# Kernel optimization log

Hardware: AMD Instinct MI355X
Metric: run time of the kernel (lower is better)

The kernel has to match this reference:

```python
import jax, jax.numpy as jnp
import numpy as np

N = 10000      # num_nodes
E = 640000     # num_edges
D = 256        # in_channels
POOL_SIZES = [(N, 48), (48, 12), (12, 4), (4, 1)]


def gcn_conv(x, src, dst, ew, W, b, n):
    """PyG-style GCNConv with edge weights: add self-loops, symmetric norm, scatter-add."""
    loop = jnp.arange(n)
    s = jnp.concatenate([src, loop])
    d = jnp.concatenate([dst, loop])
    w = jnp.concatenate([ew, jnp.ones((n,), x.dtype)])
    deg = jax.ops.segment_sum(w, d, num_segments=n)
    dinv = jnp.where(deg > 0, deg ** -0.5, 0.0)
    norm = dinv[s] * w * dinv[d]                      # [E+N]
    h = x @ W                                         # [n, out]
    out = jax.ops.segment_sum(norm[:, None] * h[s], d, num_segments=n)
    return out + b


def diffpool(x, P):
    """Learned-assignment DiffPool: S=softmax(P); x'=S^T x; reg = mean row entropy of S."""
    S = jax.nn.softmax(P, axis=-1)                    # [n_in, n_out]
    xp = S.T @ x                                      # [n_out, feat]
    reg = jnp.mean(-jnp.sum(S * jnp.log(S + 1e-12), axis=-1))
    return xp, reg


def setup_inputs() -> dict:
    key = jax.random.key(0)
    ks = jax.random.split(key, 12)
    inp = {
        "x": jax.random.normal(ks[0], (N, D), jnp.float32),
        "edge_index": jax.random.randint(ks[1], (2, E), 0, N, jnp.int64),
        "edge_attr": jax.random.uniform(ks[2], (E, 1), jnp.float32),
        "adj": jax.random.uniform(ks[3], (N, N), jnp.float32),
        # GCNConv params (out channels hard-coded to 1 in the module)
        "W1": jax.random.normal(ks[4], (D, 1), jnp.float32) / np.sqrt(D),
        "b1": jnp.zeros((1,), jnp.float32),
        "W2": jax.random.normal(ks[5], (1, 1), jnp.float32),
        "b2": jnp.zeros((1,), jnp.float32),
    }
    for i, (ni, no) in enumerate(POOL_SIZES):
        inp[f"P{i+1}"] = jax.random.normal(ks[6 + i], (ni, no), jnp.float32) * 0.1
    return inp


def reference(x, edge_index, edge_attr, adj, W1, b1, W2, b2, P1, P2, P3, P4):
    src, dst = edge_index[0], edge_index[1]
    ew = edge_attr[:, 0]
    h1 = gcn_conv(x, src, dst, ew, W1, b1, N)                       # [N,1]
    h = jnp.concatenate([h1, gcn_conv(h1[:, -1:], src, dst, ew, W2, b2, N)], axis=-1)
    h = jnp.concatenate([h, gcn_conv(h[:, -1:], src, dst, ew, W2, b2, N)], axis=-1)  # [N,3]
    reg = jnp.float32(0.0)
    for P in (P1, P2, P3, P4):
        h, r = diffpool(h, P)
        reg = reg + r
    return (h, reg)                                                  # h: [1,3]
```

## Files before the change

kernel.cpp:

```cpp
#include <hip/hip_runtime.h>
#include <math.h>

#define NN 10000
#define EE 640000
#define DD 256
#define SB 256
#define EPB (EE / SB)
#define NTHR 512
#define RB 157

#define OFF_DINV 0
#define OFF_XW   (NN)
#define OFF_C1   (2*NN)
#define OFF_C2   (3*NN)
#define OFF_U0   (4*NN)
#define OFF_U1   (5*NN)
#define OFF_U2   (6*NN)
#define OFF_XP   (7*NN)
#define OFF_PART (7*NN + 160)

__global__ __launch_bounds__(NTHR) void k1_deg_xw(
    const int* __restrict__ dst, const float* __restrict__ ew,
    const float* __restrict__ x, const float* __restrict__ W1,
    float* __restrict__ ws)
{
    __shared__ float acc[NN];
    int tid = threadIdx.x, bid = blockIdx.x;
    int lane = tid & 63, wv = tid >> 6;
    if (bid == 0 && tid < 160) ws[OFF_XP + tid] = 0.f;
    for (int i = tid; i < NN; i += NTHR) acc[i] = 0.f;
    __syncthreads();
    {
        float4 wreg = reinterpret_cast<const float4*>(W1)[lane];
        float* xw = ws + OFF_XW;
        for (int row = bid * 8 + wv; row < NN; row += SB * 8) {
            float4 a = reinterpret_cast<const float4*>(x + (size_t)row * DD)[lane];
            float v = a.x*wreg.x + a.y*wreg.y + a.z*wreg.z + a.w*wreg.w;
            #pragma unroll
            for (int off = 32; off; off >>= 1) v += __shfl_xor(v, off);
            if (lane == 0) xw[row] = v;
        }
    }
    int base = bid * EPB;
    for (int k = tid; k < EPB; k += NTHR) {
        int e = base + k;
        atomicAdd(&acc[dst[e]], ew[e]);
    }
    __syncthreads();
    float* p = ws + OFF_PART + (size_t)bid * NN;
    for (int i = tid; i < NN; i += NTHR) p[i] = acc[i];
}

__global__ __launch_bounds__(NTHR) void k2_dinv(float* __restrict__ ws)
{
    __shared__ float red[8][64];
    int tid = threadIdx.x, bid = blockIdx.x;
    int nl = tid & 63, sl = tid >> 6;
    int node = bid * 64 + nl;
    const float* part = ws + OFF_PART;
    float s = 0.f;
    if (node < NN) {
        #pragma unroll 8
        for (int it = 0; it < SB / 8; ++it)
            s += part[(size_t)(sl * (SB / 8) + it) * NN + node];
    }
    red[sl][nl] = s;
    __syncthreads();
    if (tid < 64 && node < NN) {
        float tot = 1.f;
        #pragma unroll
        for (int q = 0; q < 8; ++q) tot += red[q][tid];
        float di = (tot > 0.f) ? 1.0f / sqrtf(tot) : 0.f;
        ws[OFF_DINV + node] = di;
        ws[OFF_U0 + node] = di * ws[OFF_XW + node];
    }
}

__global__ __launch_bounds__(NTHR) void k_scat(
    const int* __restrict__ src, const int* __restrict__ dst,
    const float* __restrict__ ew, const float* __restrict__ u,
    float* __restrict__ ws)
{
    __shared__ float acc[NN];
    int tid = threadIdx.x, bid = blockIdx.x;
    for (int i = tid; i < NN; i += NTHR) acc[i] = 0.f;
    __syncthreads();
    int base = bid * EPB;
    for (int k = tid; k < EPB; k += NTHR) {
        int e = base + k;
        atomicAdd(&acc[dst[e]], ew[e] * u[src[e]]);
    }
    __syncthreads();
    float* p = ws + OFF_PART + (size_t)bid * NN;
    for (int i = tid; i < NN; i += NTHR) p[i] = acc[i];
}

__global__ __launch_bounds__(NTHR) void k_red_conv(
    const float* __restrict__ hin, const float* __restrict__ multp,
    const float* __restrict__ biasp, float* __restrict__ cout,
    float* __restrict__ uout, float* __restrict__ ws)
{
    __shared__ float red[8][64];
    int tid = threadIdx.x, bid = blockIdx.x;
    int nl = tid & 63, sl = tid >> 6;
    int node = bid * 64 + nl;
    const float* part = ws + OFF_PART;
    float s = 0.f;
    if (node < NN) {
        #pragma unroll 8
        for (int it = 0; it < SB / 8; ++it)
            s += part[(size_t)(sl * (SB / 8) + it) * NN + node];
    }
    red[sl][nl] = s;
    __syncthreads();
    if (tid < 64 && node < NN) {
        float tot = 0.f;
        #pragma unroll
        for (int q = 0; q < 8; ++q) tot += red[q][tid];
        float di = ws[OFF_DINV + node];
        float M = multp ? *multp : 1.0f;
        float cv = M * di * (tot + di * hin[node]) + *biasp;
        cout[node] = cv;
        uout[node] = di * cv;
    }
}

__global__ __launch_bounds__(NTHR) void k8_final(
    const float* __restrict__ hin,
    const float* __restrict__ multp, const float* __restrict__ biasp,
    const float* __restrict__ c1, const float* __restrict__ c2,
    const float* __restrict__ P1, const float* __restrict__ P2,
    const float* __restrict__ P3, float* __restrict__ ws, float* __restrict__ out)
{
    __shared__ float red[8][64];
    __shared__ float s_c3[64];
    __shared__ float part[8][48][3];
    __shared__ float entW[8];
    __shared__ int sh_last;
    int tid = threadIdx.x, bid = blockIdx.x;
    int lane = tid & 63, wv = tid >> 6;
    int node = bid * 64 + lane;
    const float* partg = ws + OFF_PART;
    float s = 0.f;
    if (node < NN) {
        #pragma unroll 8
        for (int it = 0; it < SB / 8; ++it)
            s += partg[(size_t)(wv * (SB / 8) + it) * NN + node];
    }
    red[wv][lane] = s;
    __syncthreads();
    if (tid < 64) {
        float cv = 0.f;
        if (node < NN) {
            float tot = 0.f;
            #pragma unroll
            for (int q = 0; q < 8; ++q) tot += red[q][tid];
            float di = ws[OFF_DINV + node];
            cv = (*multp) * di * (tot + di * hin[node]) + *biasp;
        }
        s_c3[tid] = cv;
    }
    __syncthreads();
    float a0 = 0.f, a1 = 0.f, a2 = 0.f, ent = 0.f;
    for (int j = 0; j < 8; ++j) {
        int rl = wv * 8 + j;
        int row = bid * 64 + rl;
        if (row >= NN) break;
        float v = (lane < 48) ? P1[(size_t)row * 48 + lane] : -1e30f;
        float mx = v;
        #pragma unroll
        for (int off = 32; off; off >>= 1) mx = fmaxf(mx, __shfl_xor(mx, off));
        float e = (lane < 48) ? expf(v - mx) : 0.f;
        float sum = e;
        #pragma unroll
        for (int off = 32; off; off >>= 1) sum += __shfl_xor(sum, off);
        float p = e / sum;
        if (lane < 48) {
            ent -= p * logf(p + 1e-12f);
            a0 += p * c1[row];
            a1 += p * c2[row];
            a2 += p * s_c3[rl];
        }
    }
    #pragma unroll
    for (int off = 32; off; off >>= 1) ent += __shfl_xor(ent, off);
    if (lane == 0) entW[wv] = ent;
    if (lane < 48) { part[wv][lane][0] = a0; part[wv][lane][1] = a1; part[wv][lane][2] = a2; }
    __syncthreads();
    float* xp1 = ws + OFF_XP;
    if (tid < 144) {
        int j = tid / 3, col = tid % 3;
        float sp = 0.f;
        #pragma unroll
        for (int w = 0; w < 8; ++w) sp += part[w][j][col];
        atomicAdd(&xp1[j * 3 + col], sp);
    }
    if (tid == 0) {
        float sp = 0.f;
        #pragma unroll
        for (int w = 0; w < 8; ++w) sp += entW[w];
        atomicAdd(&xp1[144], sp);
    }
    if (tid == 0) {
        __threadfence();
        int old = atomicAdd((int*)ws + OFF_XP + 152, 1);
        sh_last = (old == (int)gridDim.x - 1) ? 1 : 0;
    }
    __syncthreads();
    if (sh_last) {
        __shared__ float shXp[145];
        __shared__ float S2[48][12], xp2[12][3];
        __shared__ float S3[12][4], xp3[4][3];
        __shared__ float ent2, ent3;
        if (tid < 145) shXp[tid] = atomicAdd(&xp1[tid], 0.0f);
        if (tid == 0) { ent2 = 0.f; ent3 = 0.f; }
        __syncthreads();
        if (tid < 48) {
            float v[12], mx = -1e30f;
            #pragma unroll
            for (int j = 0; j < 12; j++) { v[j] = P2[tid * 12 + j]; mx = fmaxf(mx, v[j]); }
            float sm = 0.f;
            #pragma unroll
            for (int j = 0; j < 12; j++) { v[j] = expf(v[j] - mx); sm += v[j]; }
            float e = 0.f;
            #pragma unroll
            for (int j = 0; j < 12; j++) {
                float p = v[j] / sm; S2[tid][j] = p; e -= p * logf(p + 1e-12f);
            }
            atomicAdd(&ent2, e);
        }
        __syncthreads();
        if (tid < 36) {
            int j = tid / 3, col = tid % 3;
            float sm = 0.f;
            for (int i = 0; i < 48; i++) sm += S2[i][j] * shXp[i * 3 + col];
            xp2[j][col] = sm;
        }
        __syncthreads();
        if (tid < 12) {
            float v[4], mx = -1e30f;
            #pragma unroll
            for (int j = 0; j < 4; j++) { v[j] = P3[tid * 4 + j]; mx = fmaxf(mx, v[j]); }
            float sm = 0.f;
            #pragma unroll
            for (int j = 0; j < 4; j++) { v[j] = expf(v[j] - mx); sm += v[j]; }
            float e = 0.f;
            #pragma unroll
            for (int j = 0; j < 4; j++) {
                float p = v[j] / sm; S3[tid][j] = p; e -= p * logf(p + 1e-12f);
            }
            atomicAdd(&ent3, e);
        }
        __syncthreads();
        if (tid < 12) {
            int j = tid / 3, col = tid % 3;
            float sm = 0.f;
            for (int i = 0; i < 12; i++) sm += S3[i][j] * xp2[i][col];
            xp3[j][col] = sm;
        }
        __syncthreads();
        if (tid == 0) {
            float o0 = 0.f, o1 = 0.f, o2 = 0.f;
            for (int i = 0; i < 4; i++) {
                o0 += xp3[i][0]; o1 += xp3[i][1]; o2 += xp3[i][2];
            }
            float reg = shXp[144] / (float)NN + ent2 / 48.f + ent3 / 12.f;
            out[0] = o0; out[1] = o1; out[2] = o2; out[3] = reg;
        }
    }
}

extern "C" void kernel_launch(void* const* d_in, const int* in_sizes, int n_in,
                              void* d_out, int out_size, void* d_ws, size_t ws_size,
                              hipStream_t stream) {
    const float* x  = (const float*)d_in[0];
    const int*   ei = (const int*)d_in[1];
    const float* ea = (const float*)d_in[2];
    const float* W1 = (const float*)d_in[4];
    const float* b1 = (const float*)d_in[5];
    const float* W2 = (const float*)d_in[6];
    const float* b2 = (const float*)d_in[7];
    const float* P1 = (const float*)d_in[8];
    const float* P2 = (const float*)d_in[9];
    const float* P3 = (const float*)d_in[10];
    const int* src = ei;
    const int* dst = ei + EE;
    float* ws  = (float*)d_ws;
    float* out = (float*)d_out;

    k1_deg_xw<<<SB, NTHR, 0, stream>>>(dst, ea, x, W1, ws);
    k2_dinv<<<RB, NTHR, 0, stream>>>(ws);
    k_scat<<<SB, NTHR, 0, stream>>>(src, dst, ea, ws + OFF_U0, ws);
    k_red_conv<<<RB, NTHR, 0, stream>>>(ws + OFF_XW, nullptr, b1,
                                        ws + OFF_C1, ws + OFF_U1, ws);
    k_scat<<<SB, NTHR, 0, stream>>>(src, dst, ea, ws + OFF_U1, ws);
    k_red_conv<<<RB, NTHR, 0, stream>>>(ws + OFF_C1, W2, b2,
                                        ws + OFF_C2, ws + OFF_U2, ws);
    k_scat<<<SB, NTHR, 0, stream>>>(src, dst, ea, ws + OFF_U2, ws);
    k8_final<<<RB, NTHR, 0, stream>>>(ws + OFF_C2, W2, b2,
                                      ws + OFF_C1, ws + OFF_C2,
                                      P1, P2, P3, ws, out);
}
```

Measured before the change: 87.05 us.

## Fuse all GCN and DiffPool phases into one persistent kernel with grid barriers

Replaces the eight separate kernel launches with a single persistent kernel of 256 blocks. The phases are separated by software grid barriers built on atomic counters, and one memset zeroes the accumulators and counters. The reduction phases now cover 40 nodes per block so all 256 blocks take part, and block 0 runs the final small pooling stages after a last barrier. This removes launch gaps and inter-kernel drains, but relies on all 256 blocks being co-resident (a barrier can deadlock otherwise) and adds spin-wait barrier overhead.

```diff
diff --git a/kernel.cpp b/kernel.cpp
--- a/kernel.cpp
+++ b/kernel.cpp
@@ -4,10 +4,10 @@
 #define NN 10000
 #define EE 640000
 #define DD 256
-#define SB 256
-#define EPB (EE / SB)
+#define NBLK 256
 #define NTHR 512
-#define RB 157
+#define EPB (EE / NBLK)
+#define NPB 40
 
 #define OFF_DINV 0
 #define OFF_XW   (NN)
@@ -19,200 +19,213 @@
 #define OFF_XP   (7*NN)
 #define OFF_PART (7*NN + 160)
 
-__global__ __launch_bounds__(NTHR) void k1_deg_xw(
+__device__ __forceinline__ void gbar(int* c) {
+    __syncthreads();
+    if (threadIdx.x == 0) {
+        __hip_atomic_fetch_add(c, 1, __ATOMIC_ACQ_REL, __HIP_MEMORY_SCOPE_AGENT);
+        while (__hip_atomic_load(c, __ATOMIC_RELAXED, __HIP_MEMORY_SCOPE_AGENT) < NBLK)
+            __builtin_amdgcn_s_sleep(1);
+        __builtin_amdgcn_fence(__ATOMIC_ACQUIRE, "agent");
+    }
+    __syncthreads();
+}
+
+__global__ __launch_bounds__(NTHR) void mega2(
+    const float* __restrict__ x, const int* __restrict__ src,
     const int* __restrict__ dst, const float* __restrict__ ew,
-    const float* __restrict__ x, const float* __restrict__ W1,
-    float* __restrict__ ws)
-{
-    __shared__ float acc[NN];
-    int tid = threadIdx.x, bid = blockIdx.x;
-    int lane = tid & 63, wv = tid >> 6;
-    if (bid == 0 && tid < 160) ws[OFF_XP + tid] = 0.f;
-    for (int i = tid; i < NN; i += NTHR) acc[i] = 0.f;
-    __syncthreads();
-    {
-        float4 wreg = reinterpret_cast<const float4*>(W1)[lane];
-        float* xw = ws + OFF_XW;
-        for (int row = bid * 8 + wv; row < NN; row += SB * 8) {
-            float4 a = reinterpret_cast<const float4*>(x + (size_t)row * DD)[lane];
-            float v = a.x*wreg.x + a.y*wreg.y + a.z*wreg.z + a.w*wreg.w;
-            #pragma unroll
-            for (int off = 32; off; off >>= 1) v += __shfl_xor(v, off);
-            if (lane == 0) xw[row] = v;
-        }
-    }
-    int base = bid * EPB;
-    for (int k = tid; k < EPB; k += NTHR) {
-        int e = base + k;
-        atomicAdd(&acc[dst[e]], ew[e]);
-    }
-    __syncthreads();
-    float* p = ws + OFF_PART + (size_t)bid * NN;
-    for (int i = tid; i < NN; i += NTHR) p[i] = acc[i];
-}
-
-__global__ __launch_bounds__(NTHR) void k2_dinv(float* __restrict__ ws)
-{
-    __shared__ float red[8][64];
-    int tid = threadIdx.x, bid = blockIdx.x;
-    int nl = tid & 63, sl = tid >> 6;
-    int node = bid * 64 + nl;
-    const float* part = ws + OFF_PART;
-    float s = 0.f;
-    if (node < NN) {
-        #pragma unroll 8
-        for (int it = 0; it < SB / 8; ++it)
-            s += part[(size_t)(sl * (SB / 8) + it) * NN + node];
-    }
-    red[sl][nl] = s;
-    __syncthreads();
-    if (tid < 64 && node < NN) {
-        float tot = 1.f;
-        #pragma unroll
-        for (int q = 0; q < 8; ++q) tot += red[q][tid];
-        float di = (tot > 0.f) ? 1.0f / sqrtf(tot) : 0.f;
-        ws[OFF_DINV + node] = di;
-        ws[OFF_U0 + node] = di * ws[OFF_XW + node];
-    }
-}
-
-__global__ __launch_bounds__(NTHR) void k_scat(
-    const int* __restrict__ src, const int* __restrict__ dst,
-    const float* __restrict__ ew, const float* __restrict__ u,
-    float* __restrict__ ws)
-{
-    __shared__ float acc[NN];
-    int tid = threadIdx.x, bid = blockIdx.x;
-    for (int i = tid; i < NN; i += NTHR) acc[i] = 0.f;
-    __syncthreads();
-    int base = bid * EPB;
-    for (int k = tid; k < EPB; k += NTHR) {
-        int e = base + k;
-        atomicAdd(&acc[dst[e]], ew[e] * u[src[e]]);
-    }
-    __syncthreads();
-    float* p = ws + OFF_PART + (size_t)bid * NN;
-    for (int i = tid; i < NN; i += NTHR) p[i] = acc[i];
-}
-
-__global__ __launch_bounds__(NTHR) void k_red_conv(
-    const float* __restrict__ hin, const float* __restrict__ multp,
-    const float* __restrict__ biasp, float* __restrict__ cout,
-    float* __restrict__ uout, float* __restrict__ ws)
-{
-    __shared__ float red[8][64];
-    int tid = threadIdx.x, bid = blockIdx.x;
-    int nl = tid & 63, sl = tid >> 6;
-    int node = bid * 64 + nl;
-    const float* part = ws + OFF_PART;
-    float s = 0.f;
-    if (node < NN) {
-        #pragma unroll 8
-        for (int it = 0; it < SB / 8; ++it)
-            s += part[(size_t)(sl * (SB / 8) + it) * NN + node];
-    }
-    red[sl][nl] = s;
-    __syncthreads();
-    if (tid < 64 && node < NN) {
-        float tot = 0.f;
-        #pragma unroll
-        for (int q = 0; q < 8; ++q) tot += red[q][tid];
-        float di = ws[OFF_DINV + node];
-        float M = multp ? *multp : 1.0f;
-        float cv = M * di * (tot + di * hin[node]) + *biasp;
-        cout[node] = cv;
-        uout[node] = di * cv;
-    }
-}
-
-__global__ __launch_bounds__(NTHR) void k8_final(
-    const float* __restrict__ hin,
-    const float* __restrict__ multp, const float* __restrict__ biasp,
-    const float* __restrict__ c1, const float* __restrict__ c2,
+    const float* __restrict__ W1, const float* __restrict__ b1v,
+    const float* __restrict__ W2v, const float* __restrict__ b2v,
     const float* __restrict__ P1, const float* __restrict__ P2,
     const float* __restrict__ P3, float* __restrict__ ws, float* __restrict__ out)
 {
+    __shared__ float acc[NN];
     __shared__ float red[8][64];
-    __shared__ float s_c3[64];
+    __shared__ float s_c3[NPB];
     __shared__ float part[8][48][3];
     __shared__ float entW[8];
-    __shared__ int sh_last;
-    int tid = threadIdx.x, bid = blockIdx.x;
-    int lane = tid & 63, wv = tid >> 6;
-    int node = bid * 64 + lane;
-    const float* partg = ws + OFF_PART;
-    float s = 0.f;
-    if (node < NN) {
-        #pragma unroll 8
-        for (int it = 0; it < SB / 8; ++it)
-            s += partg[(size_t)(wv * (SB / 8) + it) * NN + node];
-    }
-    red[wv][lane] = s;
+
+    const int tid = threadIdx.x, bid = blockIdx.x;
+    const int lane = tid & 63, wv = tid >> 6;
+    const int ebase = bid * EPB;
+    const int node = bid * NPB + lane;
+    const bool nok = (lane < NPB) && (node < NN);
+
+    float* dinv_g = ws + OFF_DINV;
+    float* xw_g   = ws + OFF_XW;
+    float* c1_g   = ws + OFF_C1;
+    float* c2_g   = ws + OFF_C2;
+    float* xp1    = ws + OFF_XP;
+    int*   ctr    = (int*)(ws + OFF_XP + 148);
+    float* part_g = ws + OFF_PART;
+    float* pmy    = part_g + (size_t)bid * NN;
+
+    const float b1s = *b1v, b2s = *b2v, W2s = *W2v;
+
+    for (int i = tid; i < NN; i += NTHR) acc[i] = 0.f;
+    {
+        float4 wreg = reinterpret_cast<const float4*>(W1)[lane];
+        for (int row = bid * 8 + wv; row < NN; row += NBLK * 8) {
+            float4 a = reinterpret_cast<const float4*>(x + (size_t)row * DD)[lane];
+            float v = a.x*wreg.x + a.y*wreg.y + a.z*wreg.z + a.w*wreg.w;
+            #pragma unroll
+            for (int off = 32; off; off >>= 1) v += __shfl_xor(v, off);
+            if (lane == 0) xw_g[row] = v;
+        }
+    }
     __syncthreads();
-    if (tid < 64) {
-        float cv = 0.f;
-        if (node < NN) {
-            float tot = 0.f;
-            #pragma unroll
-            for (int q = 0; q < 8; ++q) tot += red[q][tid];
-            float di = ws[OFF_DINV + node];
-            cv = (*multp) * di * (tot + di * hin[node]) + *biasp;
-        }
-        s_c3[tid] = cv;
+    for (int k = tid; k < EPB; k += NTHR) {
+        int e = ebase + k;
+        atomicAdd(&acc[dst[e]], ew[e]);
     }
     __syncthreads();
-    float a0 = 0.f, a1 = 0.f, a2 = 0.f, ent = 0.f;
-    for (int j = 0; j < 8; ++j) {
-        int rl = wv * 8 + j;
-        int row = bid * 64 + rl;
-        if (row >= NN) break;
-        float v = (lane < 48) ? P1[(size_t)row * 48 + lane] : -1e30f;
-        float mx = v;
+    for (int i = tid; i < NN; i += NTHR) pmy[i] = acc[i];
+    gbar(&ctr[0]);
+
+    {
+        int sl = wv;
+        float s = 0.f;
+        if (nok) {
+            #pragma unroll 8
+            for (int it = 0; it < 32; ++it)
+                s += part_g[(size_t)(sl * 32 + it) * NN + node];
+        }
+        red[sl][lane] = s;
+        __syncthreads();
+        if (wv == 0 && nok) {
+            float tot = 1.f;
+            #pragma unroll
+            for (int q = 0; q < 8; ++q) tot += red[q][lane];
+            float di = (tot > 0.f) ? 1.0f / sqrtf(tot) : 0.f;
+            dinv_g[node] = di;
+            ws[OFF_U0 + node] = di * xw_g[node];
+        }
+    }
+    gbar(&ctr[1]);
+
+#define SCAT_PHASE(UOFF)                                              \
+    for (int i = tid; i < NN; i += NTHR) acc[i] = 0.f;                \
+    __syncthreads();                                                  \
+    for (int k = tid; k < EPB; k += NTHR) {                           \
+        int e = ebase + k;                                            \
+        atomicAdd(&acc[dst[e]], ew[e] * ws[(UOFF) + src[e]]);         \
+    }                                                                 \
+    __syncthreads();                                                  \
+    for (int i = tid; i < NN; i += NTHR) pmy[i] = acc[i];
+
+#define RED_PHASE(HING, M, B, COUTG, UOFF_OUT)                        \
+    {                                                                 \
+        int sl = wv;                                                  \
+        float s = 0.f;                                                \
+        if (nok) {                                                    \
+            _Pragma("unroll 8")                                       \
+            for (int it = 0; it < 32; ++it)                           \
+                s += part_g[(size_t)(sl * 32 + it) * NN + node];      \
+        }                                                             \
+        red[sl][lane] = s;                                            \
+        __syncthreads();                                              \
+        if (wv == 0 && nok) {                                         \
+            float tot = 0.f;                                          \
+            _Pragma("unroll")                                         \
+            for (int q = 0; q < 8; ++q) tot += red[q][lane];          \
+            float di = dinv_g[node];                                  \
+            float cv = (M) * di * (tot + di * (HING)[node]) + (B);    \
+            (COUTG)[node] = cv;                                       \
+            ws[(UOFF_OUT) + node] = di * cv;                          \
+        }                                                             \
+    }
+
+    SCAT_PHASE(OFF_U0)
+    gbar(&ctr[2]);
+    RED_PHASE(xw_g, 1.0f, b1s, c1_g, OFF_U1)
+    gbar(&ctr[3]);
+
+    SCAT_PHASE(OFF_U1)
+    gbar(&ctr[4]);
+    RED_PHASE(c1_g, W2s, b2s, c2_g, OFF_U2)
+    gbar(&ctr[5]);
+
+    SCAT_PHASE(OFF_U2)
+    gbar(&ctr[6]);
+
+    {
+        int sl = wv;
+        float s = 0.f;
+        if (nok) {
+            #pragma unroll 8
+            for (int it = 0; it < 32; ++it)
+                s += part_g[(size_t)(sl * 32 + it) * NN + node];
+        }
+        red[sl][lane] = s;
+        __syncthreads();
+        if (wv == 0 && lane < NPB) {
+            float cv = 0.f;
+            if (node < NN) {
+                float tot = 0.f;
+                #pragma unroll
+                for (int q = 0; q < 8; ++q) tot += red[q][lane];
+                float di = dinv_g[node];
+                cv = W2s * di * (tot + di * c2_g[node]) + b2s;
+            }
+            s_c3[lane] = cv;
+        }
+        __syncthreads();
+    }
+    {
+        float a0 = 0.f, a1 = 0.f, a2 = 0.f, ent = 0.f;
         #pragma unroll
-        for (int off = 32; off; off >>= 1) mx = fmaxf(mx, __shfl_xor(mx, off));
-        float e = (lane < 48) ? expf(v - mx) : 0.f;
-        float sum = e;
+        for (int j = 0; j < 5; ++j) {
+            int rl = wv * 5 + j;
+            int row = bid * NPB + rl;
+            if (row < NN) {
+                float pv = (lane < 48) ? P1[(size_t)row * 48 + lane] : -1e30f;
+                float mx = pv;
+                #pragma unroll
+                for (int off = 32; off; off >>= 1) mx = fmaxf(mx, __shfl_xor(mx, off));
+                float e = (lane < 48) ? expf(pv - mx) : 0.f;
+                float sum = e;
+                #pragma unroll
+                for (int off = 32; off; off >>= 1) sum += __shfl_xor(sum, off);
+                float p = e / sum;
+                if (lane < 48) {
+                    ent -= p * logf(p + 1e-12f);
+                    a0 += p * c1_g[row];
+                    a1 += p * c2_g[row];
+                    a2 += p * s_c3[rl];
+                }
+            }
+        }
         #pragma unroll
-        for (int off = 32; off; off >>= 1) sum += __shfl_xor(sum, off);
-        float p = e / sum;
-        if (lane < 48) {
-            ent -= p * logf(p + 1e-12f);
-            a0 += p * c1[row];
-            a1 += p * c2[row];
-            a2 += p * s_c3[rl];
-        }
-    }
-    #pragma unroll
-    for (int off = 32; off; off >>= 1) ent += __shfl_xor(ent, off);
-    if (lane == 0) entW[wv] = ent;
-    if (lane < 48) { part[wv][lane][0] = a0; part[wv][lane][1] = a1; part[wv][lane][2] = a2; }
-    __syncthreads();
-    float* xp1 = ws + OFF_XP;
-    if (tid < 144) {
-        int j = tid / 3, col = tid % 3;
-        float sp = 0.f;
-        #pragma unroll
-        for (int w = 0; w < 8; ++w) sp += part[w][j][col];
-        atomicAdd(&xp1[j * 3 + col], sp);
-    }
-    if (tid == 0) {
-        float sp = 0.f;
-        #pragma unroll
-        for (int w = 0; w < 8; ++w) sp += entW[w];
-        atomicAdd(&xp1[144], sp);
-    }
-    if (tid == 0) {
-        __threadfence();
-        int old = atomicAdd((int*)ws + OFF_XP + 152, 1);
-        sh_last = (old == (int)gridDim.x - 1) ? 1 : 0;
-    }
-    __syncthreads();
-    if (sh_last) {
-        __shared__ float shXp[145];
+        for (int off = 32; off; off >>= 1) ent += __shfl_xor(ent, off);
+        if (lane == 0) entW[wv] = ent;
+        if (lane < 48) { part[wv][lane][0] = a0; part[wv][lane][1] = a1; part[wv][lane][2] = a2; }
+        __syncthreads();
+        if (tid < 144) {
+            int j = tid / 3, col = tid % 3;
+            float sp = 0.f;
+            #pragma unroll
+            for (int w = 0; w < 8; ++w) sp += part[w][j][col];
+            atomicAdd(&xp1[j * 3 + col], sp);
+        }
+        if (tid == 0) {
+            float sp = 0.f;
+            #pragma unroll
+            for (int w = 0; w < 8; ++w) sp += entW[w];
+            atomicAdd(&xp1[144], sp);
+        }
+    }
+
+    if (bid != 0) {
+        __syncthreads();
+        if (tid == 0)
+            __hip_atomic_fetch_add(&ctr[7], 1, __ATOMIC_RELEASE, __HIP_MEMORY_SCOPE_AGENT);
+        return;
+    }
+    gbar(&ctr[7]);
+
+    {
         __shared__ float S2[48][12], xp2[12][3];
         __shared__ float S3[12][4], xp3[4][3];
         __shared__ float ent2, ent3;
-        if (tid < 145) shXp[tid] = atomicAdd(&xp1[tid], 0.0f);
         if (tid == 0) { ent2 = 0.f; ent3 = 0.f; }
         __syncthreads();
         if (tid < 48) {
@@ -233,7 +246,7 @@
         if (tid < 36) {
             int j = tid / 3, col = tid % 3;
             float sm = 0.f;
-            for (int i = 0; i < 48; i++) sm += S2[i][j] * shXp[i * 3 + col];
+            for (int i = 0; i < 48; i++) sm += S2[i][j] * xp1[i * 3 + col];
             xp2[j][col] = sm;
         }
         __syncthreads();
@@ -264,7 +277,7 @@
             for (int i = 0; i < 4; i++) {
                 o0 += xp3[i][0]; o1 += xp3[i][1]; o2 += xp3[i][2];
             }
-            float reg = shXp[144] / (float)NN + ent2 / 48.f + ent3 / 12.f;
+            float reg = xp1[144] / (float)NN + ent2 / 48.f + ent3 / 12.f;
             out[0] = o0; out[1] = o1; out[2] = o2; out[3] = reg;
         }
     }
@@ -288,16 +301,7 @@
     float* ws  = (float*)d_ws;
     float* out = (float*)d_out;
 
-    k1_deg_xw<<<SB, NTHR, 0, stream>>>(dst, ea, x, W1, ws);
-    k2_dinv<<<RB, NTHR, 0, stream>>>(ws);
-    k_scat<<<SB, NTHR, 0, stream>>>(src, dst, ea, ws + OFF_U0, ws);
-    k_red_conv<<<RB, NTHR, 0, stream>>>(ws + OFF_XW, nullptr, b1,
-                                        ws + OFF_C1, ws + OFF_U1, ws);
-    k_scat<<<SB, NTHR, 0, stream>>>(src, dst, ea, ws + OFF_U1, ws);
-    k_red_conv<<<RB, NTHR, 0, stream>>>(ws + OFF_C1, W2, b2,
-                                        ws + OFF_C2, ws + OFF_U2, ws);
-    k_scat<<<SB, NTHR, 0, stream>>>(src, dst, ea, ws + OFF_U2, ws);
-    k8_final<<<RB, NTHR, 0, stream>>>(ws + OFF_C2, W2, b2,
-                                      ws + OFF_C1, ws + OFF_C2,
-                                      P1, P2, P3, ws, out);
+    hipMemsetAsync(ws + OFF_XP, 0, 160 * sizeof(float), stream);
+    mega2<<<NBLK, NTHR, 0, stream>>>(x, src, dst, ea, W1, b1, W2, b2,
+                                     P1, P2, P3, ws, out);
 }
```

Measured after the change: 198.7 us. 128% more time.

## Bucket edges by source block and fuse reductions into subsequent scatter kernels

Applied to the files above, without the earlier changes.

The first kernel now counting-sorts each edge chunk into 64 source-node buckets, packing the destination, local source index and weight into one 8-byte record. It also computes x@W1 and degree partials in the same pass. Each later kernel reduces the previous layer's partial sums for its own 157 nodes, computes the scaled source values in shared memory, and scatters only its bucket's edges. This cuts the launch count from eight to five and the partial-sum buffers from 256 to 64 copies. The cost is that the scatter phases run on only 64 blocks, each reading 256 small segments, which may underuse the GPU.

```diff
diff --git a/kernel.cpp b/kernel.cpp
--- a/kernel.cpp
+++ b/kernel.cpp
@@ -4,182 +4,208 @@
 #define NN 10000
 #define EE 640000
 #define DD 256
-#define SB 256
-#define EPB (EE / SB)
+#define NW 256
+#define EPW (EE / NW)
+#define NB 64
+#define NPB 157
 #define NTHR 512
-#define RB 157
+#define DEGB 64
+#define EPD (EE / DEGB)
 
 #define OFF_DINV 0
 #define OFF_XW   (NN)
 #define OFF_C1   (2*NN)
 #define OFF_C2   (3*NN)
-#define OFF_U0   (4*NN)
-#define OFF_U1   (5*NN)
-#define OFF_U2   (6*NN)
-#define OFF_XP   (7*NN)
-#define OFF_PART (7*NN + 160)
-
-__global__ __launch_bounds__(NTHR) void k1_deg_xw(
-    const int* __restrict__ dst, const float* __restrict__ ew,
-    const float* __restrict__ x, const float* __restrict__ W1,
-    float* __restrict__ ws)
-{
-    __shared__ float acc[NN];
+#define OFF_XP   (4*NN)
+#define OFF_BND  (4*NN + 160)
+#define OFF_S1   (OFF_BND + NW*65)
+#define OFF_DEGP (OFF_S1 + 2*EE)
+#define OFF_PART (OFF_DEGP + (size_t)DEGB*NN)
+
+__global__ __launch_bounds__(NTHR) void k1_sort_xw_deg(
+    const int* __restrict__ src, const int* __restrict__ dst,
+    const float* __restrict__ ew, const float* __restrict__ x,
+    const float* __restrict__ W1, float* __restrict__ ws)
+{
+    __shared__ int   sSrc[EPW], sDst[EPW];
+    __shared__ float sEw[EPW];
+    __shared__ int   cnt[NB], pf[NB + 1], curs[NB];
+    __shared__ float accD[NN];
     int tid = threadIdx.x, bid = blockIdx.x;
     int lane = tid & 63, wv = tid >> 6;
     if (bid == 0 && tid < 160) ws[OFF_XP + tid] = 0.f;
-    for (int i = tid; i < NN; i += NTHR) acc[i] = 0.f;
-    __syncthreads();
+    if (tid < NB) cnt[tid] = 0;
+    __syncthreads();
+    int base = bid * EPW;
+    for (int k = tid; k < EPW; k += NTHR) {
+        int s = src[base + k], d = dst[base + k];
+        sSrc[k] = s; sDst[k] = d; sEw[k] = ew[base + k];
+        atomicAdd(&cnt[s / NPB], 1);
+    }
+    __syncthreads();
+    if (tid < NB) {
+        int v = cnt[tid];
+        int incl = v;
+        #pragma unroll
+        for (int off = 1; off < 64; off <<= 1) {
+            int t = __shfl_up(incl, off);
+            if (lane >= off) incl += t;
+        }
+        int excl = incl - v;
+        pf[tid] = excl; curs[tid] = excl;
+        if (tid == NB - 1) pf[NB] = incl;
+    }
+    __syncthreads();
+    int* bndp = (int*)ws + OFF_BND;
+    if (tid < NB + 1) bndp[bid * 65 + tid] = pf[tid];
+    uint2* S1 = (uint2*)(ws + OFF_S1);
+    for (int k = tid; k < EPW; k += NTHR) {
+        int s = sSrc[k];
+        int j = s / NPB, loc = s - j * NPB;
+        int pos = atomicAdd(&curs[j], 1);
+        uint2 pk;
+        pk.x = (unsigned)sDst[k] | ((unsigned)loc << 14);
+        pk.y = __float_as_uint(sEw[k]);
+        S1[bid * EPW + pos] = pk;
+    }
     {
         float4 wreg = reinterpret_cast<const float4*>(W1)[lane];
-        float* xw = ws + OFF_XW;
-        for (int row = bid * 8 + wv; row < NN; row += SB * 8) {
-            float4 a = reinterpret_cast<const float4*>(x + (size_t)row * DD)[lane];
-            float v = a.x*wreg.x + a.y*wreg.y + a.z*wreg.z + a.w*wreg.w;
-            #pragma unroll
-            for (int off = 32; off; off >>= 1) v += __shfl_xor(v, off);
-            if (lane == 0) xw[row] = v;
-        }
-    }
-    int base = bid * EPB;
-    for (int k = tid; k < EPB; k += NTHR) {
-        int e = base + k;
-        atomicAdd(&acc[dst[e]], ew[e]);
-    }
-    __syncthreads();
-    float* p = ws + OFF_PART + (size_t)bid * NN;
-    for (int i = tid; i < NN; i += NTHR) p[i] = acc[i];
-}
-
-__global__ __launch_bounds__(NTHR) void k2_dinv(float* __restrict__ ws)
-{
-    __shared__ float red[8][64];
+        #pragma unroll
+        for (int r = 0; r < 5; ++r) {
+            int row = bid * 40 + wv * 5 + r;
+            if (row < NN) {
+                float4 a = reinterpret_cast<const float4*>(x + (size_t)row * DD)[lane];
+                float v = a.x*wreg.x + a.y*wreg.y + a.z*wreg.z + a.w*wreg.w;
+                #pragma unroll
+                for (int off = 32; off; off >>= 1) v += __shfl_xor(v, off);
+                if (lane == 0) ws[OFF_XW + row] = v;
+            }
+        }
+    }
+    if (bid < DEGB) {
+        for (int i = tid; i < NN; i += NTHR) accD[i] = 0.f;
+        __syncthreads();
+        int b2 = bid * EPD;
+        for (int k = tid; k < EPD; k += NTHR)
+            atomicAdd(&accD[dst[b2 + k]], ew[b2 + k]);
+        __syncthreads();
+        float* dp = ws + OFF_DEGP + (size_t)bid * NN;
+        for (int i = tid; i < NN; i += NTHR) dp[i] = accD[i];
+    }
+}
+
+__device__ __forceinline__ void bucket_scatter(
+    const int* bndp, const uint2* S1, const float* du, float* acc, int bid,
+    int lane, int wv)
+{
+    for (int w = wv; w < NW; w += 8) {
+        int s = bndp[w * 65 + bid], e = bndp[w * 65 + bid + 1];
+        for (int k = s + lane; k < e; k += 64) {
+            uint2 pk = S1[w * EPW + k];
+            atomicAdd(&acc[pk.x & 0x3FFF], __uint_as_float(pk.y) * du[pk.x >> 14]);
+        }
+    }
+}
+
+__global__ __launch_bounds__(NTHR) void k2_dinv_conv1(float* __restrict__ ws)
+{
+    __shared__ float acc[NN];
+    __shared__ float du[NPB];
     int tid = threadIdx.x, bid = blockIdx.x;
-    int nl = tid & 63, sl = tid >> 6;
-    int node = bid * 64 + nl;
-    const float* part = ws + OFF_PART;
-    float s = 0.f;
-    if (node < NN) {
-        #pragma unroll 8
-        for (int it = 0; it < SB / 8; ++it)
-            s += part[(size_t)(sl * (SB / 8) + it) * NN + node];
-    }
-    red[sl][nl] = s;
-    __syncthreads();
-    if (tid < 64 && node < NN) {
-        float tot = 1.f;
-        #pragma unroll
-        for (int q = 0; q < 8; ++q) tot += red[q][tid];
-        float di = (tot > 0.f) ? 1.0f / sqrtf(tot) : 0.f;
-        ws[OFF_DINV + node] = di;
-        ws[OFF_U0 + node] = di * ws[OFF_XW + node];
-    }
-}
-
-__global__ __launch_bounds__(NTHR) void k_scat(
-    const int* __restrict__ src, const int* __restrict__ dst,
-    const float* __restrict__ ew, const float* __restrict__ u,
+    int lane = tid & 63, wv = tid >> 6;
+    int nbase = bid * NPB;
+    int ncnt = min(NPB, NN - nbase);
+    for (int i = tid; i < NN; i += NTHR) acc[i] = 0.f;
+    if (tid < ncnt) {
+        float s = 1.f;
+        const float* dp = ws + OFF_DEGP;
+        for (int w = 0; w < DEGB; ++w) s += dp[(size_t)w * NN + nbase + tid];
+        float di = (s > 0.f) ? 1.0f / sqrtf(s) : 0.f;
+        ws[OFF_DINV + nbase + tid] = di;
+        du[tid] = di * ws[OFF_XW + nbase + tid];
+    }
+    __syncthreads();
+    bucket_scatter((const int*)ws + OFF_BND, (const uint2*)(ws + OFF_S1),
+                   du, acc, bid, lane, wv);
+    __syncthreads();
+    float* pp = ws + OFF_PART + (size_t)bid * NN;
+    for (int i = tid; i < NN; i += NTHR) pp[i] = acc[i];
+}
+
+__global__ __launch_bounds__(NTHR) void k_conv(
+    const float* __restrict__ hing, const float* __restrict__ multp,
+    const float* __restrict__ biasp, float* __restrict__ cout,
+    const float* __restrict__ pin, float* __restrict__ pout,
     float* __restrict__ ws)
 {
     __shared__ float acc[NN];
+    __shared__ float du[NPB];
     int tid = threadIdx.x, bid = blockIdx.x;
+    int lane = tid & 63, wv = tid >> 6;
+    int nbase = bid * NPB;
+    int ncnt = min(NPB, NN - nbase);
     for (int i = tid; i < NN; i += NTHR) acc[i] = 0.f;
-    __syncthreads();
-    int base = bid * EPB;
-    for (int k = tid; k < EPB; k += NTHR) {
-        int e = base + k;
-        atomicAdd(&acc[dst[e]], ew[e] * u[src[e]]);
-    }
-    __syncthreads();
-    float* p = ws + OFF_PART + (size_t)bid * NN;
-    for (int i = tid; i < NN; i += NTHR) p[i] = acc[i];
-}
-
-__global__ __launch_bounds__(NTHR) void k_red_conv(
-    const float* __restrict__ hin, const float* __restrict__ multp,
-    const float* __restrict__ biasp, float* __restrict__ cout,
-    float* __restrict__ uout, float* __restrict__ ws)
-{
-    __shared__ float red[8][64];
-    int tid = threadIdx.x, bid = blockIdx.x;
-    int nl = tid & 63, sl = tid >> 6;
-    int node = bid * 64 + nl;
-    const float* part = ws + OFF_PART;
-    float s = 0.f;
-    if (node < NN) {
-        #pragma unroll 8
-        for (int it = 0; it < SB / 8; ++it)
-            s += part[(size_t)(sl * (SB / 8) + it) * NN + node];
-    }
-    red[sl][nl] = s;
-    __syncthreads();
-    if (tid < 64 && node < NN) {
-        float tot = 0.f;
-        #pragma unroll
-        for (int q = 0; q < 8; ++q) tot += red[q][tid];
-        float di = ws[OFF_DINV + node];
+    if (tid < ncnt) {
+        float s = 0.f;
+        for (int w = 0; w < NB; ++w) s += pin[(size_t)w * NN + nbase + tid];
+        float di = ws[OFF_DINV + nbase + tid];
         float M = multp ? *multp : 1.0f;
-        float cv = M * di * (tot + di * hin[node]) + *biasp;
-        cout[node] = cv;
-        uout[node] = di * cv;
-    }
-}
-
-__global__ __launch_bounds__(NTHR) void k8_final(
-    const float* __restrict__ hin,
+        float cv = M * di * (s + di * hing[nbase + tid]) + *biasp;
+        cout[nbase + tid] = cv;
+        du[tid] = di * cv;
+    }
+    __syncthreads();
+    bucket_scatter((const int*)ws + OFF_BND, (const uint2*)(ws + OFF_S1),
+                   du, acc, bid, lane, wv);
+    __syncthreads();
+    float* pp = pout + (size_t)bid * NN;
+    for (int i = tid; i < NN; i += NTHR) pp[i] = acc[i];
+}
+
+__global__ __launch_bounds__(NTHR) void k5_final(
     const float* __restrict__ multp, const float* __restrict__ biasp,
-    const float* __restrict__ c1, const float* __restrict__ c2,
+    const float* __restrict__ pin,
     const float* __restrict__ P1, const float* __restrict__ P2,
     const float* __restrict__ P3, float* __restrict__ ws, float* __restrict__ out)
 {
-    __shared__ float red[8][64];
-    __shared__ float s_c3[64];
+    __shared__ float sc3[NPB];
     __shared__ float part[8][48][3];
     __shared__ float entW[8];
     __shared__ int sh_last;
     int tid = threadIdx.x, bid = blockIdx.x;
     int lane = tid & 63, wv = tid >> 6;
-    int node = bid * 64 + lane;
-    const float* partg = ws + OFF_PART;
-    float s = 0.f;
-    if (node < NN) {
-        #pragma unroll 8
-        for (int it = 0; it < SB / 8; ++it)
-            s += partg[(size_t)(wv * (SB / 8) + it) * NN + node];
-    }
-    red[wv][lane] = s;
-    __syncthreads();
-    if (tid < 64) {
-        float cv = 0.f;
-        if (node < NN) {
-            float tot = 0.f;
-            #pragma unroll
-            for (int q = 0; q < 8; ++q) tot += red[q][tid];
-            float di = ws[OFF_DINV + node];
-            cv = (*multp) * di * (tot + di * hin[node]) + *biasp;
-        }
-        s_c3[tid] = cv;
+    int nbase = bid * NPB;
+    int ncnt = min(NPB, NN - nbase);
+    const float* c1 = ws + OFF_C1;
+    const float* c2 = ws + OFF_C2;
+    if (tid < ncnt) {
+        float s = 0.f;
+        for (int w = 0; w < NB; ++w) s += pin[(size_t)w * NN + nbase + tid];
+        float di = ws[OFF_DINV + nbase + tid];
+        float cv = (*multp) * di * (s + di * c2[nbase + tid]) + *biasp;
+        sc3[tid] = cv;
     }
     __syncthreads();
     float a0 = 0.f, a1 = 0.f, a2 = 0.f, ent = 0.f;
-    for (int j = 0; j < 8; ++j) {
-        int rl = wv * 8 + j;
-        int row = bid * 64 + rl;
-        if (row >= NN) break;
-        float v = (lane < 48) ? P1[(size_t)row * 48 + lane] : -1e30f;
-        float mx = v;
-        #pragma unroll
-        for (int off = 32; off; off >>= 1) mx = fmaxf(mx, __shfl_xor(mx, off));
-        float e = (lane < 48) ? expf(v - mx) : 0.f;
-        float sum = e;
-        #pragma unroll
-        for (int off = 32; off; off >>= 1) sum += __shfl_xor(sum, off);
-        float p = e / sum;
-        if (lane < 48) {
-            ent -= p * logf(p + 1e-12f);
-            a0 += p * c1[row];
-            a1 += p * c2[row];
-            a2 += p * s_c3[rl];
+    for (int r = 0; r < 20; ++r) {
+        int l = wv * 20 + r;
+        if (l < ncnt) {
+            int row = nbase + l;
+            float pv = (lane < 48) ? P1[(size_t)row * 48 + lane] : -1e30f;
+            float mx = pv;
+            #pragma unroll
+            for (int off = 32; off; off >>= 1) mx = fmaxf(mx, __shfl_xor(mx, off));
+            float e = (lane < 48) ? expf(pv - mx) : 0.f;
+            float sum = e;
+            #pragma unroll
+            for (int off = 32; off; off >>= 1) sum += __shfl_xor(sum, off);
+            float p = e / sum;
+            if (lane < 48) {
+                ent -= p * logf(p + 1e-12f);
+                a0 += p * c1[row];
+                a1 += p * c2[row];
+                a2 += p * sc3[l];
+            }
         }
     }
     #pragma unroll
@@ -288,16 +314,15 @@
     float* ws  = (float*)d_ws;
     float* out = (float*)d_out;
 
-    k1_deg_xw<<<SB, NTHR, 0, stream>>>(dst, ea, x, W1, ws);
-    k2_dinv<<<RB, NTHR, 0, stream>>>(ws);
-    k_scat<<<SB, NTHR, 0, stream>>>(src, dst, ea, ws + OFF_U0, ws);
-    k_red_conv<<<RB, NTHR, 0, stream>>>(ws + OFF_XW, nullptr, b1,
-                                        ws + OFF_C1, ws + OFF_U1, ws);
-    k_scat<<<SB, NTHR, 0, stream>>>(src, dst, ea, ws + OFF_U1, ws);
-    k_red_conv<<<RB, NTHR, 0, stream>>>(ws + OFF_C1, W2, b2,
-                                        ws + OFF_C2, ws + OFF_U2, ws);
-    k_scat<<<SB, NTHR, 0, stream>>>(src, dst, ea, ws + OFF_U2, ws);
-    k8_final<<<RB, NTHR, 0, stream>>>(ws + OFF_C2, W2, b2,
-                                      ws + OFF_C1, ws + OFF_C2,
-                                      P1, P2, P3, ws, out);
-}
+    float* xw    = ws + OFF_XW;
+    float* c1    = ws + OFF_C1;
+    float* c2    = ws + OFF_C2;
+    float* partA = ws + OFF_PART;
+    float* partB = ws + OFF_DEGP;
+
+    k1_sort_xw_deg<<<NW, NTHR, 0, stream>>>(src, dst, ea, x, W1, ws);
+    k2_dinv_conv1<<<NB, NTHR, 0, stream>>>(ws);
+    k_conv<<<NB, NTHR, 0, stream>>>(xw, nullptr, b1, c1, partA, partB, ws);
+    k_conv<<<NB, NTHR, 0, stream>>>(c1, W2, b2, c2, partB, partA, ws);
+    k5_final<<<NB, NTHR, 0, stream>>>(W2, b2, partA, P1, P2, P3, ws, out);
+}
```

New measurement: 125.7 us. 1.44x slower.
